# Performance work log

Hardware: AMD Instinct MI355X
Metric: run time of the kernel (lower is better)

Reference implementation:

```python
import jax, jax.numpy as jnp
import numpy as np

DEPTH = 11  # tree depth -> depth+1 routing steps, n_nodes = 2**(DEPTH+1)-1 = 4095


def setup_inputs() -> dict:
    key = jax.random.key(0)
    k1, k2, k3 = jax.random.split(key, 3)
    B, D_in, D_out = 8192, 2048, 2048
    n_nodes = 2 ** (DEPTH + 1) - 1
    x = jax.random.normal(k1, (B, D_in), dtype=jnp.float32)
    # nn.Linear(input_width, n_nodes, bias=False).weight : (n_nodes, D_in)
    W_in = jax.random.normal(k2, (n_nodes, D_in), dtype=jnp.float32) / np.sqrt(D_in).astype(np.float32)
    # nn.Linear(n_nodes, output_width, bias=False).weight : (D_out, n_nodes)
    W_out = jax.random.normal(k3, (D_out, n_nodes), dtype=jnp.float32) / np.sqrt(n_nodes).astype(np.float32)
    return {"x": x, "W_in": W_in, "W_out": W_out}


def reference(x, W_in, W_out):
    B = x.shape[0]
    # Torch loop recomputes linear_in(x) every step; the result is identical each
    # iteration, so compute the (B, n_nodes) logits once and gather per depth step.
    logits_all = x @ W_in.T  # (B, n_nodes)

    def step(cur, _):
        # gather the logit of each sample's current tree node
        score = jnp.take_along_axis(logits_all, cur[:, None], axis=1)[:, 0]  # (B,)
        nxt = cur * 2 + (score >= 0).astype(jnp.int32) + 1  # left/right child
        return nxt, (cur, score)

    init = jnp.zeros((B,), dtype=jnp.int32)
    _, (nodes, scores) = jax.lax.scan(step, init, None, length=DEPTH + 1)
    nodes = nodes.T    # (B, depth+1) visited node ids
    scores = scores.T  # (B, depth+1) selected logits

    mlp1 = jax.nn.gelu(scores, approximate=False)  # exact GELU, matches nn.GELU
    # Conditional output projection: only the depth+1 visited columns of W_out
    # contribute per sample (FFF / conditional-MoE semantics).
    W_sel = W_out.T[nodes]  # (B, depth+1, D_out)
    return jnp.einsum('bd,bdo->bo', mlp1, W_sel)
```

## Files before the change

### kernel.cpp

```cpp
#include <hip/hip_runtime.h>
#include <math.h>

#define B_SZ     8192
#define D_IN     2048
#define D_OUT    2048
#define N_NODES  4095
#define STEPS    12
#define N_LEAVES 2048
#define N_SUB    512
#define CAP      64

typedef float f4 __attribute__((ext_vector_type(4)));

__device__ __forceinline__ f4 nt_load(const float* p) {
  return __builtin_nontemporal_load((const f4*)p);
}

__global__ __launch_bounds__(256, 5) void route_tr_kernel(
    const float* __restrict__ x, const float* __restrict__ W_in,
    const float* __restrict__ W_out, float* __restrict__ Wt,
    int* __restrict__ cnt, int* __restrict__ bucket,
    float* __restrict__ gsc) {
  __shared__ float tile[64][65];
  const int tid = threadIdx.x;

  {
    const int wave = (int)(blockIdx.x * 4 + (tid >> 6));
    const int lane = tid & 63;

    const float* xbase = x + (size_t)wave * D_IN;
    f4 xv0 = nt_load(xbase + (lane + 0 * 64) * 4);
    f4 xv1 = nt_load(xbase + (lane + 1 * 64) * 4);
    f4 xv2 = nt_load(xbase + (lane + 2 * 64) * 4);
    f4 xv3 = nt_load(xbase + (lane + 3 * 64) * 4);
    f4 xv4 = nt_load(xbase + (lane + 4 * 64) * 4);
    f4 xv5 = nt_load(xbase + (lane + 5 * 64) * 4);
    f4 xv6 = nt_load(xbase + (lane + 6 * 64) * 4);
    f4 xv7 = nt_load(xbase + (lane + 7 * 64) * 4);
    asm volatile("" : "+v"(xv0), "+v"(xv1), "+v"(xv2), "+v"(xv3),
                      "+v"(xv4), "+v"(xv5), "+v"(xv6), "+v"(xv7));

    int cur = 0;
    #pragma unroll
    for (int d = 0; d < STEPS; ++d) {
      const f4* wr = (const f4*)(W_in + (size_t)cur * D_IN);
      f4 w0 = wr[lane + 0 * 64];
      f4 w1 = wr[lane + 1 * 64];
      f4 w2 = wr[lane + 2 * 64];
      f4 w3 = wr[lane + 3 * 64];
      f4 w4 = wr[lane + 4 * 64];
      f4 w5 = wr[lane + 5 * 64];
      f4 w6 = wr[lane + 6 * 64];
      f4 w7 = wr[lane + 7 * 64];
      asm volatile("" : "+v"(w0), "+v"(w1), "+v"(w2), "+v"(w3),
                        "+v"(w4), "+v"(w5), "+v"(w6), "+v"(w7));
      float s = 0.0f;
      s += xv0.x * w0.x + xv0.y * w0.y + xv0.z * w0.z + xv0.w * w0.w;
      s += xv1.x * w1.x + xv1.y * w1.y + xv1.z * w1.z + xv1.w * w1.w;
      s += xv2.x * w2.x + xv2.y * w2.y + xv2.z * w2.z + xv2.w * w2.w;
      s += xv3.x * w3.x + xv3.y * w3.y + xv3.z * w3.z + xv3.w * w3.w;
      s += xv4.x * w4.x + xv4.y * w4.y + xv4.z * w4.z + xv4.w * w4.w;
      s += xv5.x * w5.x + xv5.y * w5.y + xv5.z * w5.z + xv5.w * w5.w;
      s += xv6.x * w6.x + xv6.y * w6.y + xv6.z * w6.z + xv6.w * w6.w;
      s += xv7.x * w7.x + xv7.y * w7.y + xv7.z * w7.z + xv7.w * w7.w;

      #pragma unroll
      for (int off = 32; off > 0; off >>= 1) s += __shfl_xor(s, off);

      if (lane == 0) {
        gsc[wave * STEPS + d] = 0.5f * s * (1.0f + erff(s * 0.70710678118654752f));
        if (d == STEPS - 1) {
          const int leaf = cur - 2047;
          const int pos = atomicAdd(&cnt[leaf], 1);
          if (pos < CAP) bucket[leaf * CAP + pos] = wave;
        }
      }
      cur = cur * 2 + ((s >= 0.0f) ? 2 : 1);
    }
  }

  {
    const int bx = blockIdx.x;
    const int col0 = (bx & 63) * 64;
    const int row0 = (bx >> 6) * 64;
    const int r  = tid >> 4;
    const int c4 = (tid & 15) * 4;

    #pragma unroll
    for (int i = 0; i < 4; ++i) {
      const int row = r + i * 16;
      const float* src = W_out + (size_t)(row0 + row) * N_NODES + col0 + c4;
      if (col0 + c4 + 3 < N_NODES) {
        const f4 v = nt_load(src);
        tile[c4 + 0][row] = v.x; tile[c4 + 1][row] = v.y;
        tile[c4 + 2][row] = v.z; tile[c4 + 3][row] = v.w;
      } else {
        #pragma unroll
        for (int k = 0; k < 4; ++k)
          tile[c4 + k][row] = (col0 + c4 + k < N_NODES) ? src[k] : 0.0f;
      }
    }
    __syncthreads();
    #pragma unroll
    for (int i = 0; i < 4; ++i) {
      const int rn = r + i * 16;
      const int node = col0 + rn;
      if (node < N_NODES) {
        float4 v;
        v.x = tile[rn][c4 + 0]; v.y = tile[rn][c4 + 1];
        v.z = tile[rn][c4 + 2]; v.w = tile[rn][c4 + 3];
        *(float4*)(Wt + (size_t)node * D_OUT + row0 + c4) = v;
      }
    }
  }
}

__global__ __launch_bounds__(256) void out_kernel(
    const float* __restrict__ Wt, const int* __restrict__ cnt,
    const int* __restrict__ bucket, const float* __restrict__ gsc,
    float* __restrict__ out) {
  const int sub = blockIdx.x * 4 + (threadIdx.x >> 6);
  const int lane = threadIdx.x & 63;
  const int col = blockIdx.y * 256 + lane * 4;

  int anc[10];
  {
    int nd = 511 + sub;
    #pragma unroll
    for (int d = 9; d >= 0; --d) { anc[d] = nd; nd = (nd - 1) >> 1; }
  }
  const int p10a = 1023 + 2 * sub;
  const int leaf0n = 2047 + 4 * sub;

  f4 wa0 = *(const f4*)(Wt + (size_t)anc[0] * D_OUT + col);
  f4 wa1 = *(const f4*)(Wt + (size_t)anc[1] * D_OUT + col);
  f4 wa2 = *(const f4*)(Wt + (size_t)anc[2] * D_OUT + col);
  f4 wa3 = *(const f4*)(Wt + (size_t)anc[3] * D_OUT + col);
  f4 wa4 = *(const f4*)(Wt + (size_t)anc[4] * D_OUT + col);
  f4 wa5 = *(const f4*)(Wt + (size_t)anc[5] * D_OUT + col);
  f4 wa6 = *(const f4*)(Wt + (size_t)anc[6] * D_OUT + col);
  f4 wa7 = *(const f4*)(Wt + (size_t)anc[7] * D_OUT + col);
  f4 wa8 = *(const f4*)(Wt + (size_t)anc[8] * D_OUT + col);
  f4 wa9 = *(const f4*)(Wt + (size_t)anc[9] * D_OUT + col);
  f4 wp0 = *(const f4*)(Wt + (size_t)(p10a + 0) * D_OUT + col);
  f4 wp1 = *(const f4*)(Wt + (size_t)(p10a + 1) * D_OUT + col);
  f4 wl0 = *(const f4*)(Wt + (size_t)(leaf0n + 0) * D_OUT + col);
  f4 wl1 = *(const f4*)(Wt + (size_t)(leaf0n + 1) * D_OUT + col);
  f4 wl2 = *(const f4*)(Wt + (size_t)(leaf0n + 2) * D_OUT + col);
  f4 wl3 = *(const f4*)(Wt + (size_t)(leaf0n + 3) * D_OUT + col);
  asm volatile("" : "+v"(wa0), "+v"(wa1), "+v"(wa2), "+v"(wa3), "+v"(wa4),
                    "+v"(wa5), "+v"(wa6), "+v"(wa7), "+v"(wa8), "+v"(wa9),
                    "+v"(wp0), "+v"(wp1),
                    "+v"(wl0), "+v"(wl1), "+v"(wl2), "+v"(wl3));

  int n0 = cnt[4 * sub + 0]; if (n0 > CAP) n0 = CAP;
  int n1 = cnt[4 * sub + 1]; if (n1 > CAP) n1 = CAP;
  int n2 = cnt[4 * sub + 2]; if (n2 > CAP) n2 = CAP;
  int n3 = cnt[4 * sub + 3]; if (n3 > CAP) n3 = CAP;
  const int p1 = n0, p2 = n0 + n1, p3 = n0 + n1 + n2;
  const int total = p3 + n3;

  for (int base = 0; base < total; base += 64) {
    const int m = (total - base < 64) ? (total - base) : 64;
    int packed = 0;
    {
      const int gi = base + lane;
      if (gi < total) {
        int lc, off;
        if      (gi < p1) { lc = 0; off = 0;  }
        else if (gi < p2) { lc = 1; off = p1; }
        else if (gi < p3) { lc = 2; off = p2; }
        else              { lc = 3; off = p3; }
        const int b = bucket[(4 * sub + lc) * CAP + (gi - off)];
        packed = (lc << 28) | b;
      }
    }
    int pA = __shfl(packed, 0);
    int pB = __shfl(packed, (m > 1) ? 1 : 0);
    const float4* gA = (const float4*)(gsc + (size_t)(pA & 0x0FFFFFFF) * STEPS);
    float4 a0 = gA[0], a1 = gA[1], a2 = gA[2];
    const float4* gB = (const float4*)(gsc + (size_t)(pB & 0x0FFFFFFF) * STEPS);
    float4 b0 = gB[0], b1 = gB[1], b2 = gB[2];

    for (int j = 0; j < m; ++j) {
      int jn = j + 2; if (jn >= m) jn = m - 1;
      const int pC = __shfl(packed, jn);
      const float4* gC = (const float4*)(gsc + (size_t)(pC & 0x0FFFFFFF) * STEPS);
      const float4 t0 = gC[0], t1 = gC[1], t2 = gC[2];

      const int b  = pA & 0x0FFFFFFF;
      const int lc = pA >> 28;
      const f4 w10 = (lc & 2) ? wp1 : wp0;
      const f4 w11 = (lc & 2) ? ((lc & 1) ? wl3 : wl2)
                              : ((lc & 1) ? wl1 : wl0);
      f4 acc;
      acc.x = a0.x * wa0.x; acc.y = a0.x * wa0.y;
      acc.z = a0.x * wa0.z; acc.w = a0.x * wa0.w;
      acc.x += a0.y * wa1.x; acc.y += a0.y * wa1.y;
      acc.z += a0.y * wa1.z; acc.w += a0.y * wa1.w;
      acc.x += a0.z * wa2.x; acc.y += a0.z * wa2.y;
      acc.z += a0.z * wa2.z; acc.w += a0.z * wa2.w;
      acc.x += a0.w * wa3.x; acc.y += a0.w * wa3.y;
      acc.z += a0.w * wa3.z; acc.w += a0.w * wa3.w;
      acc.x += a1.x * wa4.x; acc.y += a1.x * wa4.y;
      acc.z += a1.x * wa4.z; acc.w += a1.x * wa4.w;
      acc.x += a1.y * wa5.x; acc.y += a1.y * wa5.y;
      acc.z += a1.y * wa5.z; acc.w += a1.y * wa5.w;
      acc.x += a1.z * wa6.x; acc.y += a1.z * wa6.y;
      acc.z += a1.z * wa6.z; acc.w += a1.z * wa6.w;
      acc.x += a1.w * wa7.x; acc.y += a1.w * wa7.y;
      acc.z += a1.w * wa7.z; acc.w += a1.w * wa7.w;
      acc.x += a2.x * wa8.x; acc.y += a2.x * wa8.y;
      acc.z += a2.x * wa8.z; acc.w += a2.x * wa8.w;
      acc.x += a2.y * wa9.x; acc.y += a2.y * wa9.y;
      acc.z += a2.y * wa9.z; acc.w += a2.y * wa9.w;
      acc.x += a2.z * w10.x; acc.y += a2.z * w10.y;
      acc.z += a2.z * w10.z; acc.w += a2.z * w10.w;
      acc.x += a2.w * w11.x; acc.y += a2.w * w11.y;
      acc.z += a2.w * w11.z; acc.w += a2.w * w11.w;
      __builtin_nontemporal_store(acc, (f4*)(out + (size_t)b * D_OUT + col));

      pA = pB; a0 = b0; a1 = b1; a2 = b2;
      pB = pC; b0 = t0; b1 = t1; b2 = t2;
    }
  }
}

extern "C" void kernel_launch(void* const* d_in, const int* in_sizes, int n_in,
                              void* d_out, int out_size, void* d_ws, size_t ws_size,
                              hipStream_t stream) {
  const float* x     = (const float*)d_in[0];
  const float* W_in  = (const float*)d_in[1];
  const float* W_out = (const float*)d_in[2];
  float* out = (float*)d_out;

  char* p = (char*)d_ws;
  float* Wt     = (float*)p;  p += (size_t)N_NODES * D_OUT * sizeof(float);
  int*   cnt    = (int*)p;    p += (size_t)N_LEAVES * sizeof(int);
  int*   bucket = (int*)p;    p += (size_t)N_LEAVES * CAP * sizeof(int);
  float* gsc    = (float*)p;

  hipMemsetAsync(cnt, 0, (size_t)N_LEAVES * sizeof(int), stream);

  route_tr_kernel<<<dim3(2048), dim3(256), 0, stream>>>(
      x, W_in, W_out, Wt, cnt, bucket, gsc);

  out_kernel<<<dim3(N_SUB / 4, 8), dim3(256), 0, stream>>>(
      Wt, cnt, bucket, gsc, out);
}
```

Baseline: 221.7 us.

## Fuse memset, routing, transpose and output into one cooperative kernel

Replaces the memset plus two kernel launches with a single cooperative kernel of 1024 blocks that zeroes the leaf counters, routes two samples per wave, transposes W_out, and then computes the output, using grid-wide syncs between phases. This removes launch overheads and the gaps between kernels. The cost is grid.sync barriers and a smaller grid that does twice the work per block, with occupancy lowered to 4 blocks per CU. If the cooperative launch fails, the code falls back to the original three-step path.

```diff
diff --git a/kernel.cpp b/kernel.cpp
--- a/kernel.cpp
+++ b/kernel.cpp
@@ -1,5 +1,8 @@
 #include <hip/hip_runtime.h>
+#include <hip/hip_cooperative_groups.h>
 #include <math.h>
+
+namespace cg = cooperative_groups;
 
 #define B_SZ     8192
 #define D_IN     2048
@@ -9,6 +12,7 @@
 #define N_LEAVES 2048
 #define N_SUB    512
 #define CAP      64
+#define GRID_BLKS 1024
 
 typedef float f4 __attribute__((ext_vector_type(4)));
 
@@ -16,17 +20,28 @@
   return __builtin_nontemporal_load((const f4*)p);
 }
 
-__global__ __launch_bounds__(256, 5) void route_tr_kernel(
+__global__ __launch_bounds__(256, 4) void fff_all(
     const float* __restrict__ x, const float* __restrict__ W_in,
     const float* __restrict__ W_out, float* __restrict__ Wt,
     int* __restrict__ cnt, int* __restrict__ bucket,
-    float* __restrict__ gsc) {
+    float* __restrict__ gsc, float* __restrict__ out) {
   __shared__ float tile[64][65];
-  const int tid = threadIdx.x;
+  cg::grid_group grid = cg::this_grid();
+  const int tid  = threadIdx.x;
+  const int bid  = blockIdx.x;
+  const int wid  = tid >> 6;
+  const int lane = tid & 63;
 
   {
-    const int wave = (int)(blockIdx.x * 4 + (tid >> 6));
-    const int lane = tid & 63;
+    const int i = bid * 256 + tid;
+    if (i < N_LEAVES) cnt[i] = 0;
+  }
+  __threadfence();
+  grid.sync();
+
+  #pragma unroll 1
+  for (int rep = 0; rep < 2; ++rep) {
+    const int wave = bid * 8 + wid * 2 + rep;
 
     const float* xbase = x + (size_t)wave * D_IN;
     f4 xv0 = nt_load(xbase + (lane + 0 * 64) * 4);
@@ -79,6 +94,217 @@
     }
   }
 
+  #pragma unroll 1
+  for (int t = 0; t < 2; ++t) {
+    const int bx = bid + t * GRID_BLKS;
+    const int col0 = (bx & 63) * 64;
+    const int row0 = (bx >> 6) * 64;
+    const int r  = tid >> 4;
+    const int c4 = (tid & 15) * 4;
+
+    if (t) __syncthreads();
+    #pragma unroll
+    for (int i = 0; i < 4; ++i) {
+      const int row = r + i * 16;
+      const float* src = W_out + (size_t)(row0 + row) * N_NODES + col0 + c4;
+      if (col0 + c4 + 3 < N_NODES) {
+        const f4 v = nt_load(src);
+        tile[c4 + 0][row] = v.x; tile[c4 + 1][row] = v.y;
+        tile[c4 + 2][row] = v.z; tile[c4 + 3][row] = v.w;
+      } else {
+        #pragma unroll
+        for (int k = 0; k < 4; ++k)
+          tile[c4 + k][row] = (col0 + c4 + k < N_NODES) ? src[k] : 0.0f;
+      }
+    }
+    __syncthreads();
+    #pragma unroll
+    for (int i = 0; i < 4; ++i) {
+      const int rn = r + i * 16;
+      const int node = col0 + rn;
+      if (node < N_NODES) {
+        float4 v;
+        v.x = tile[rn][c4 + 0]; v.y = tile[rn][c4 + 1];
+        v.z = tile[rn][c4 + 2]; v.w = tile[rn][c4 + 3];
+        *(float4*)(Wt + (size_t)node * D_OUT + row0 + c4) = v;
+      }
+    }
+  }
+
+  __threadfence();
+  grid.sync();
+
+  {
+    const int subgrp  = bid & 127;
+    const int coltile = bid >> 7;
+    const int sub = subgrp * 4 + wid;
+    const int col = coltile * 256 + lane * 4;
+
+    int anc[10];
+    {
+      int nd = 511 + sub;
+      #pragma unroll
+      for (int d = 9; d >= 0; --d) { anc[d] = nd; nd = (nd - 1) >> 1; }
+    }
+    const int p10a = 1023 + 2 * sub;
+    const int leaf0n = 2047 + 4 * sub;
+
+    f4 wa0 = *(const f4*)(Wt + (size_t)anc[0] * D_OUT + col);
+    f4 wa1 = *(const f4*)(Wt + (size_t)anc[1] * D_OUT + col);
+    f4 wa2 = *(const f4*)(Wt + (size_t)anc[2] * D_OUT + col);
+    f4 wa3 = *(const f4*)(Wt + (size_t)anc[3] * D_OUT + col);
+    f4 wa4 = *(const f4*)(Wt + (size_t)anc[4] * D_OUT + col);
+    f4 wa5 = *(const f4*)(Wt + (size_t)anc[5] * D_OUT + col);
+    f4 wa6 = *(const f4*)(Wt + (size_t)anc[6] * D_OUT + col);
+    f4 wa7 = *(const f4*)(Wt + (size_t)anc[7] * D_OUT + col);
+    f4 wa8 = *(const f4*)(Wt + (size_t)anc[8] * D_OUT + col);
+    f4 wa9 = *(const f4*)(Wt + (size_t)anc[9] * D_OUT + col);
+    f4 wp0 = *(const f4*)(Wt + (size_t)(p10a + 0) * D_OUT + col);
+    f4 wp1 = *(const f4*)(Wt + (size_t)(p10a + 1) * D_OUT + col);
+    f4 wl0 = *(const f4*)(Wt + (size_t)(leaf0n + 0) * D_OUT + col);
+    f4 wl1 = *(const f4*)(Wt + (size_t)(leaf0n + 1) * D_OUT + col);
+    f4 wl2 = *(const f4*)(Wt + (size_t)(leaf0n + 2) * D_OUT + col);
+    f4 wl3 = *(const f4*)(Wt + (size_t)(leaf0n + 3) * D_OUT + col);
+    asm volatile("" : "+v"(wa0), "+v"(wa1), "+v"(wa2), "+v"(wa3), "+v"(wa4),
+                      "+v"(wa5), "+v"(wa6), "+v"(wa7), "+v"(wa8), "+v"(wa9),
+                      "+v"(wp0), "+v"(wp1),
+                      "+v"(wl0), "+v"(wl1), "+v"(wl2), "+v"(wl3));
+
+    int n0 = cnt[4 * sub + 0]; if (n0 > CAP) n0 = CAP;
+    int n1 = cnt[4 * sub + 1]; if (n1 > CAP) n1 = CAP;
+    int n2 = cnt[4 * sub + 2]; if (n2 > CAP) n2 = CAP;
+    int n3 = cnt[4 * sub + 3]; if (n3 > CAP) n3 = CAP;
+    const int p1 = n0, p2 = n0 + n1, p3 = n0 + n1 + n2;
+    const int total = p3 + n3;
+
+    for (int base = 0; base < total; base += 64) {
+      const int m = (total - base < 64) ? (total - base) : 64;
+      int packed = 0;
+      {
+        const int gi = base + lane;
+        if (gi < total) {
+          int lc, off;
+          if      (gi < p1) { lc = 0; off = 0;  }
+          else if (gi < p2) { lc = 1; off = p1; }
+          else if (gi < p3) { lc = 2; off = p2; }
+          else              { lc = 3; off = p3; }
+          const int b = bucket[(4 * sub + lc) * CAP + (gi - off)];
+          packed = (lc << 28) | b;
+        }
+      }
+      int pA = __shfl(packed, 0);
+      int pB = __shfl(packed, (m > 1) ? 1 : 0);
+      const float4* gA = (const float4*)(gsc + (size_t)(pA & 0x0FFFFFFF) * STEPS);
+      float4 a0 = gA[0], a1 = gA[1], a2 = gA[2];
+      const float4* gB = (const float4*)(gsc + (size_t)(pB & 0x0FFFFFFF) * STEPS);
+      float4 b0 = gB[0], b1 = gB[1], b2 = gB[2];
+
+      for (int j = 0; j < m; ++j) {
+        int jn = j + 2; if (jn >= m) jn = m - 1;
+        const int pC = __shfl(packed, jn);
+        const float4* gC = (const float4*)(gsc + (size_t)(pC & 0x0FFFFFFF) * STEPS);
+        const float4 t0 = gC[0], t1 = gC[1], t2 = gC[2];
+
+        const int b  = pA & 0x0FFFFFFF;
+        const int lc = pA >> 28;
+        const f4 w10 = (lc & 2) ? wp1 : wp0;
+        const f4 w11 = (lc & 2) ? ((lc & 1) ? wl3 : wl2)
+                                : ((lc & 1) ? wl1 : wl0);
+        f4 acc;
+        acc.x = a0.x * wa0.x; acc.y = a0.x * wa0.y;
+        acc.z = a0.x * wa0.z; acc.w = a0.x * wa0.w;
+        acc.x += a0.y * wa1.x; acc.y += a0.y * wa1.y;
+        acc.z += a0.y * wa1.z; acc.w += a0.y * wa1.w;
+        acc.x += a0.z * wa2.x; acc.y += a0.z * wa2.y;
+        acc.z += a0.z * wa2.z; acc.w += a0.z * wa2.w;
+        acc.x += a0.w * wa3.x; acc.y += a0.w * wa3.y;
+        acc.z += a0.w * wa3.z; acc.w += a0.w * wa3.w;
+        acc.x += a1.x * wa4.x; acc.y += a1.x * wa4.y;
+        acc.z += a1.x * wa4.z; acc.w += a1.x * wa4.w;
+        acc.x += a1.y * wa5.x; acc.y += a1.y * wa5.y;
+        acc.z += a1.y * wa5.z; acc.w += a1.y * wa5.w;
+        acc.x += a1.z * wa6.x; acc.y += a1.z * wa6.y;
+        acc.z += a1.z * wa6.z; acc.w += a1.z * wa6.w;
+        acc.x += a1.w * wa7.x; acc.y += a1.w * wa7.y;
+        acc.z += a1.w * wa7.z; acc.w += a1.w * wa7.w;
+        acc.x += a2.x * wa8.x; acc.y += a2.x * wa8.y;
+        acc.z += a2.x * wa8.z; acc.w += a2.x * wa8.w;
+        acc.x += a2.y * wa9.x; acc.y += a2.y * wa9.y;
+        acc.z += a2.y * wa9.z; acc.w += a2.y * wa9.w;
+        acc.x += a2.z * w10.x; acc.y += a2.z * w10.y;
+        acc.z += a2.z * w10.z; acc.w += a2.z * w10.w;
+        acc.x += a2.w * w11.x; acc.y += a2.w * w11.y;
+        acc.z += a2.w * w11.z; acc.w += a2.w * w11.w;
+        __builtin_nontemporal_store(acc, (f4*)(out + (size_t)b * D_OUT + col));
+
+        pA = pB; a0 = b0; a1 = b1; a2 = b2;
+        pB = pC; b0 = t0; b1 = t1; b2 = t2;
+      }
+    }
+  }
+}
+
+__global__ __launch_bounds__(256, 5) void route_tr_kernel(
+    const float* __restrict__ x, const float* __restrict__ W_in,
+    const float* __restrict__ W_out, float* __restrict__ Wt,
+    int* __restrict__ cnt, int* __restrict__ bucket,
+    float* __restrict__ gsc) {
+  __shared__ float tile[64][65];
+  const int tid = threadIdx.x;
+  {
+    const int wave = (int)(blockIdx.x * 4 + (tid >> 6));
+    const int lane = tid & 63;
+
+    const float* xbase = x + (size_t)wave * D_IN;
+    f4 xv0 = nt_load(xbase + (lane + 0 * 64) * 4);
+    f4 xv1 = nt_load(xbase + (lane + 1 * 64) * 4);
+    f4 xv2 = nt_load(xbase + (lane + 2 * 64) * 4);
+    f4 xv3 = nt_load(xbase + (lane + 3 * 64) * 4);
+    f4 xv4 = nt_load(xbase + (lane + 4 * 64) * 4);
+    f4 xv5 = nt_load(xbase + (lane + 5 * 64) * 4);
+    f4 xv6 = nt_load(xbase + (lane + 6 * 64) * 4);
+    f4 xv7 = nt_load(xbase + (lane + 7 * 64) * 4);
+    asm volatile("" : "+v"(xv0), "+v"(xv1), "+v"(xv2), "+v"(xv3),
+                      "+v"(xv4), "+v"(xv5), "+v"(xv6), "+v"(xv7));
+
+    int cur = 0;
+    #pragma unroll
+    for (int d = 0; d < STEPS; ++d) {
+      const f4* wr = (const f4*)(W_in + (size_t)cur * D_IN);
+      f4 w0 = wr[lane + 0 * 64];
+      f4 w1 = wr[lane + 1 * 64];
+      f4 w2 = wr[lane + 2 * 64];
+      f4 w3 = wr[lane + 3 * 64];
+      f4 w4 = wr[lane + 4 * 64];
+      f4 w5 = wr[lane + 5 * 64];
+      f4 w6 = wr[lane + 6 * 64];
+      f4 w7 = wr[lane + 7 * 64];
+      asm volatile("" : "+v"(w0), "+v"(w1), "+v"(w2), "+v"(w3),
+                        "+v"(w4), "+v"(w5), "+v"(w6), "+v"(w7));
+      float s = 0.0f;
+      s += xv0.x * w0.x + xv0.y * w0.y + xv0.z * w0.z + xv0.w * w0.w;
+      s += xv1.x * w1.x + xv1.y * w1.y + xv1.z * w1.z + xv1.w * w1.w;
+      s += xv2.x * w2.x + xv2.y * w2.y + xv2.z * w2.z + xv2.w * w2.w;
+      s += xv3.x * w3.x + xv3.y * w3.y + xv3.z * w3.z + xv3.w * w3.w;
+      s += xv4.x * w4.x + xv4.y * w4.y + xv4.z * w4.z + xv4.w * w4.w;
+      s += xv5.x * w5.x + xv5.y * w5.y + xv5.z * w5.z + xv5.w * w5.w;
+      s += xv6.x * w6.x + xv6.y * w6.y + xv6.z * w6.z + xv6.w * w6.w;
+      s += xv7.x * w7.x + xv7.y * w7.y + xv7.z * w7.z + xv7.w * w7.w;
+
+      #pragma unroll
+      for (int off = 32; off > 0; off >>= 1) s += __shfl_xor(s, off);
+
+      if (lane == 0) {
+        gsc[wave * STEPS + d] = 0.5f * s * (1.0f + erff(s * 0.70710678118654752f));
+        if (d == STEPS - 1) {
+          const int leaf = cur - 2047;
+          const int pos = atomicAdd(&cnt[leaf], 1);
+          if (pos < CAP) bucket[leaf * CAP + pos] = wave;
+        }
+      }
+      cur = cur * 2 + ((s >= 0.0f) ? 2 : 1);
+    }
+  }
   {
     const int bx = blockIdx.x;
     const int col0 = (bx & 63) * 64;
@@ -240,11 +466,17 @@
   int*   bucket = (int*)p;    p += (size_t)N_LEAVES * CAP * sizeof(int);
   float* gsc    = (float*)p;
 
-  hipMemsetAsync(cnt, 0, (size_t)N_LEAVES * sizeof(int), stream);
-
-  route_tr_kernel<<<dim3(2048), dim3(256), 0, stream>>>(
-      x, W_in, W_out, Wt, cnt, bucket, gsc);
-
-  out_kernel<<<dim3(N_SUB / 4, 8), dim3(256), 0, stream>>>(
-      Wt, cnt, bucket, gsc, out);
+  void* args[] = {(void*)&x, (void*)&W_in, (void*)&W_out, (void*)&Wt,
+                  (void*)&cnt, (void*)&bucket, (void*)&gsc, (void*)&out};
+  hipError_t e = hipLaunchCooperativeKernel(
+      (const void*)fff_all, dim3(GRID_BLKS), dim3(256), args, 0, stream);
+
+  if (e != hipSuccess) {
+    (void)hipGetLastError();
+    hipMemsetAsync(cnt, 0, (size_t)N_LEAVES * sizeof(int), stream);
+    route_tr_kernel<<<dim3(2048), dim3(256), 0, stream>>>(
+        x, W_in, W_out, Wt, cnt, bucket, gsc);
+    out_kernel<<<dim3(N_SUB / 4, 8), dim3(256), 0, stream>>>(
+        Wt, cnt, bucket, gsc, out);
+  }
 }
```

New measurement: 597.5 us. +169.5%, slower.
